# Optimization experiments

Measured on AMD Instinct MI355X. Metric: run time of the kernel, lower is better.

The kernel has to match this reference:

```python
import jax, jax.numpy as jnp
import numpy as np

N, H, E, A, T = 50000, 128, 800000, 16, 4


def setup_inputs() -> dict:
    key = jax.random.key(0)
    ks = jax.random.split(key, 12)
    s = 1.0 / np.sqrt(H + A)
    s2 = 1.0 / np.sqrt(H)
    return {
        "h": jax.random.normal(ks[0], (N, H), dtype=jnp.float32),
        "edge_index": jax.random.randint(ks[1], (2, E), 0, N, dtype=jnp.int32),
        "edge_type": jax.random.randint(ks[2], (E,), 0, T, dtype=jnp.int32),
        "edge_attr": jax.random.normal(ks[3], (E, A), dtype=jnp.float32),
        # per-edge-type 2-layer MLP params
        "W1": jax.random.uniform(ks[4], (T, H + A, H), minval=-s, maxval=s, dtype=jnp.float32),
        "b1": jax.random.uniform(ks[5], (T, H), minval=-s, maxval=s, dtype=jnp.float32),
        "W2": jax.random.uniform(ks[6], (T, H, H), minval=-s2, maxval=s2, dtype=jnp.float32),
        "b2": jax.random.uniform(ks[7], (T, H), minval=-s2, maxval=s2, dtype=jnp.float32),
        # GRUCell params (torch layout: [3H, H] with gate order r, z, n)
        "w_ih": jax.random.uniform(ks[8], (3 * H, H), minval=-s2, maxval=s2, dtype=jnp.float32),
        "w_hh": jax.random.uniform(ks[9], (3 * H, H), minval=-s2, maxval=s2, dtype=jnp.float32),
        "b_ih": jax.random.uniform(ks[10], (3 * H,), minval=-s2, maxval=s2, dtype=jnp.float32),
        "b_hh": jax.random.uniform(ks[11], (3 * H,), minval=-s2, maxval=s2, dtype=jnp.float32),
    }


def reference(h, edge_index, edge_type, edge_attr, W1, b1, W2, b2, w_ih, w_hh, b_ih, b_hh):
    src, dst = edge_index[0], edge_index[1]
    h_in = jnp.concatenate([h[src], edge_attr], axis=-1)  # [E, H+A]
    # per-edge-type MLP; loop over small fixed num_edge_types, mask-select
    m = jnp.zeros((h_in.shape[0], H), dtype=h.dtype)
    for t in range(T):
        mt = jax.nn.relu(h_in @ W1[t] + b1[t]) @ W2[t] + b2[t]  # [E, H]
        m = jnp.where((edge_type == t)[:, None], mt, m)
    # scatter-add messages to destination nodes
    msg = jax.ops.segment_sum(m, dst, num_segments=h.shape[0])  # [N, H]
    # GRUCell(msg, h) with torch gate order r, z, n
    gi = msg @ w_ih.T + b_ih  # [N, 3H]
    gh = h @ w_hh.T + b_hh
    i_r, i_z, i_n = jnp.split(gi, 3, axis=-1)
    h_r, h_z, h_n = jnp.split(gh, 3, axis=-1)
    r = jax.nn.sigmoid(i_r + h_r)
    z = jax.nn.sigmoid(i_z + h_z)
    n = jnp.tanh(i_n + r * h_n)
    return (1.0 - z) * n + z * h
```

## Files before the change

### kernel.cpp

```cpp
#include <hip/hip_runtime.h>
#include <stdint.h>

#define Hh 128
#define Aa 16
#define Tt 4
#define K1 144
#define K1P 160
#define W1T_LD 168
#define WG_LD  136

typedef float f32x4 __attribute__((ext_vector_type(4)));
typedef __bf16 bf16x8 __attribute__((ext_vector_type(8)));
typedef unsigned short u16x8 __attribute__((ext_vector_type(8)));
typedef unsigned short u16x4 __attribute__((ext_vector_type(4)));

static __device__ __forceinline__ unsigned short f2bf(float f) {
    unsigned u = __builtin_bit_cast(unsigned, f);
    u += 0x7fffu + ((u >> 16) & 1u);
    return (unsigned short)(u >> 16);
}

static __device__ __forceinline__ float bf2f(unsigned short u) {
    return __builtin_bit_cast(float, (unsigned)u << 16);
}

static __device__ __forceinline__ bf16x8 zero_bf8() {
    u16x8 z = {0, 0, 0, 0, 0, 0, 0, 0};
    return __builtin_bit_cast(bf16x8, z);
}

__global__ void cast_all_kernel(
    const float* __restrict__ h, const float* __restrict__ ea,
    const float* __restrict__ wih, const float* __restrict__ whh,
    unsigned short* __restrict__ h_bf, unsigned short* __restrict__ ebf,
    unsigned short* __restrict__ wihb, unsigned short* __restrict__ whhb,
    int n0, int n1, int n2, int n3)
{
    int i = blockIdx.x * blockDim.x + threadIdx.x;
    if (i >= n3) return;
    const float* s; unsigned short* d; int off;
    if (i < n0)      { s = h;   d = h_bf; off = i; }
    else if (i < n1) { s = ea;  d = ebf;  off = i - n0; }
    else if (i < n2) { s = wih; d = wihb; off = i - n1; }
    else             { s = whh; d = whhb; off = i - n2; }
    f32x4 v = *(const f32x4*)(s + (size_t)off * 4);
    u16x4 o;
    o[0] = f2bf(v[0]); o[1] = f2bf(v[1]); o[2] = f2bf(v[2]); o[3] = f2bf(v[3]);
    *(u16x4*)(d + (size_t)off * 4) = o;
}

__global__ void w1t_kernel(const float* __restrict__ W1, unsigned short* __restrict__ W1Tbf) {
    __shared__ float tile[16][129];
    const int b = blockIdx.x;
    const int t = b / 10, kb = b % 10;
    const int k0 = kb * 16;
    const int tid = threadIdx.x;
    for (int e = tid; e < 16 * 128; e += 256) {
        int k = e >> 7, n = e & 127;
        tile[k][n] = (k0 + k < K1) ? W1[((size_t)t * K1 + k0 + k) * Hh + n] : 0.f;
    }
    __syncthreads();
    for (int e = tid; e < 128 * 16; e += 256) {
        int n = e >> 4, kk = e & 15;
        W1Tbf[((size_t)t * Hh + n) * K1P + k0 + kk] = f2bf(tile[kk][n]);
    }
}

__global__ void w2t_kernel(const float* __restrict__ W2, unsigned short* __restrict__ W2Tbf) {
    __shared__ float tile[16][129];
    const int b = blockIdx.x;
    const int t = b >> 3, kb = b & 7;
    const int k0 = kb * 16;
    const int tid = threadIdx.x;
    for (int e = tid; e < 16 * 128; e += 256) {
        int k = e >> 7, n = e & 127;
        tile[k][n] = W2[((size_t)t * Hh + k0 + k) * Hh + n];
    }
    __syncthreads();
    for (int e = tid; e < 128 * 16; e += 256) {
        int n = e >> 4, kk = e & 15;
        W2Tbf[((size_t)t * Hh + n) * Hh + k0 + kk] = f2bf(tile[kk][n]);
    }
}

__global__ void hist_kernel(const int* __restrict__ et, const int* __restrict__ eidx,
                            int E, int N, int* __restrict__ cnt, unsigned* __restrict__ rank) {
    for (int i = blockIdx.x * blockDim.x + threadIdx.x; i < E; i += gridDim.x * blockDim.x) {
        rank[i] = (unsigned)atomicAdd(&cnt[et[i] * N + eidx[E + i]], 1);
    }
}

__global__ void scanA_kernel(const int* __restrict__ deg2, int nb, int* __restrict__ bsum) {
    __shared__ int red[256];
    const int t = threadIdx.x;
    const int i0 = blockIdx.x * 1024 + t * 4;
    int s = 0;
    #pragma unroll
    for (int j = 0; j < 4; j++) if (i0 + j < nb) s += deg2[i0 + j];
    red[t] = s; __syncthreads();
    for (int d = 128; d > 0; d >>= 1) {
        if (t < d) red[t] += red[t + d];
        __syncthreads();
    }
    if (t == 0) bsum[blockIdx.x] = red[0];
}

__global__ void scanB_kernel(int* __restrict__ bsum, int nblocks,
                             int* __restrict__ rowptrD, int fourN, int E) {
    __shared__ int ts[512];
    const int t = threadIdx.x;
    int v = (t < nblocks) ? bsum[t] : 0;
    ts[t] = v; __syncthreads();
    for (int d = 1; d < 512; d <<= 1) {
        int x = (t >= d) ? ts[t - d] : 0;
        __syncthreads();
        ts[t] += x;
        __syncthreads();
    }
    if (t < nblocks) bsum[t] = ts[t] - v;
    if (t == 0) rowptrD[fourN] = E;
}

__global__ void scanC_kernel(int* __restrict__ cur, int nb,
                             const int* __restrict__ bsum, int* __restrict__ rowptrD) {
    __shared__ int ts[256];
    const int t = threadIdx.x;
    const int i0 = blockIdx.x * 1024 + t * 4;
    int v[4];
    #pragma unroll
    for (int j = 0; j < 4; j++) v[j] = (i0 + j < nb) ? cur[i0 + j] : 0;
    int s = v[0] + v[1] + v[2] + v[3];
    ts[t] = s; __syncthreads();
    for (int d = 1; d < 256; d <<= 1) {
        int x = (t >= d) ? ts[t - d] : 0;
        __syncthreads();
        ts[t] += x;
        __syncthreads();
    }
    int run = bsum[blockIdx.x] + ts[t] - s;
    #pragma unroll
    for (int j = 0; j < 4; j++) {
        if (i0 + j < nb) {
            rowptrD[i0 + j] = run;
            cur[i0 + j] = run;
            run += v[j];
        }
    }
}

__global__ void fill2_kernel(const int* __restrict__ et, const int* __restrict__ eidx,
                             int E, int N, const int* __restrict__ binstart,
                             const unsigned* __restrict__ rank, int2* __restrict__ rec) {
    for (int i = blockIdx.x * blockDim.x + threadIdx.x; i < E; i += gridDim.x * blockDim.x) {
        int posD = binstart[et[i] * N + eidx[E + i]] + (int)rank[i];
        rec[posD] = make_int2(eidx[i], i);
    }
}

__global__ __launch_bounds__(512) void l1_kernel(
    const unsigned short* __restrict__ h_bf, const int2* __restrict__ rec,
    const unsigned short* __restrict__ ebf, const unsigned short* __restrict__ W1Tbf,
    const float* __restrict__ b1, const int* __restrict__ rowptrD,
    unsigned short* __restrict__ Yg, int N)
{
    __shared__ unsigned short W1T[128 * W1T_LD];
    __shared__ float b1s[128];
    const int tid = threadIdx.x;

    int rem = blockIdx.x, t = 0, tstart = 0, tend = 0;
    for (; t < Tt; t++) {
        tstart = rowptrD[t * N];
        tend = rowptrD[(t + 1) * N];
        int ntt = (tend - tstart + 255) >> 8;
        if (rem < ntt) break;
        rem -= ntt;
    }
    if (t == Tt) return;

    for (int idx = tid; idx < (Hh * K1P) / 8; idx += 512) {
        int n = idx / 20, c = (idx % 20) * 8;
        *(u16x8*)&W1T[n * W1T_LD + c] =
            *(const u16x8*)&W1Tbf[((size_t)t * Hh + n) * K1P + c];
    }
    if (tid < 128) b1s[tid] = b1[t * Hh + tid];
    __syncthreads();

    const int w = tid >> 6, lane = tid & 63;
    const int l15 = lane & 15, q = lane >> 4;
    const int tl = tend - 1;

    const int p0 = tstart + rem * 256 + w * 32;
    const int pa = p0 + l15, pb = p0 + 16 + l15;
    const bool va = pa < tend, vb = pb < tend;
    const int2 ra = rec[min(pa, tl)];
    const int2 rb = rec[min(pb, tl)];
    const unsigned short* __restrict__ hA = h_bf + (size_t)ra.x * Hh;
    const unsigned short* __restrict__ hB = h_bf + (size_t)rb.x * Hh;

    f32x4 acc[8][2];
    #pragma unroll
    for (int mt = 0; mt < 8; mt++) {
        acc[mt][0] = (f32x4){0.f, 0.f, 0.f, 0.f};
        acc[mt][1] = (f32x4){0.f, 0.f, 0.f, 0.f};
    }

    #pragma unroll
    for (int ks = 0; ks < 5; ks++) {
        const int k0 = ks * 32;
        bf16x8 fb_a, fb_b;
        if (ks < 4) {
            fb_a = __builtin_bit_cast(bf16x8, *(const u16x8*)(hA + k0 + q * 8));
            fb_b = __builtin_bit_cast(bf16x8, *(const u16x8*)(hB + k0 + q * 8));
        } else if (q < 2) {
            fb_a = __builtin_bit_cast(bf16x8, *(const u16x8*)(ebf + (size_t)ra.y * Aa + q * 8));
            fb_b = __builtin_bit_cast(bf16x8, *(const u16x8*)(ebf + (size_t)rb.y * Aa + q * 8));
        } else {
            fb_a = zero_bf8();
            fb_b = zero_bf8();
        }
        #pragma unroll
        for (int mt = 0; mt < 8; mt++) {
            bf16x8 fa = *(const bf16x8*)&W1T[(mt * 16 + l15) * W1T_LD + k0 + q * 8];
            acc[mt][0] = __builtin_amdgcn_mfma_f32_16x16x32_bf16(fa, fb_a, acc[mt][0], 0, 0, 0);
            acc[mt][1] = __builtin_amdgcn_mfma_f32_16x16x32_bf16(fa, fb_b, acc[mt][1], 0, 0, 0);
        }
    }

    #pragma unroll
    for (int g = 0; g < 2; g++) {
        if (g ? vb : va) {
            unsigned short* __restrict__ o = Yg + (size_t)(g ? pb : pa) * Hh + q * 4;
            #pragma unroll
            for (int mt = 0; mt < 8; mt++) {
                f32x4 bias = *(const f32x4*)&b1s[mt * 16 + q * 4];
                u16x4 y;
                #pragma unroll
                for (int i = 0; i < 4; i++) {
                    float v = acc[mt][g][i] + bias[i];
                    y[i] = f2bf(v > 0.f ? v : 0.f);
                }
                *(u16x4*)(o + mt * 16) = y;
            }
        }
    }
}

__global__ __launch_bounds__(256) void zgemm_kernel(
    const unsigned short* __restrict__ Yg, const int* __restrict__ rowptrD,
    const unsigned short* __restrict__ W2Tbf, const float* __restrict__ b2,
    unsigned short* __restrict__ msgb, int N)
{
    __shared__ unsigned short W2T[128 * WG_LD];
    __shared__ float b2s[512];
    __shared__ int cntS[4 * 64];
    const int tid = threadIdx.x;
    const int w = tid >> 6, lane = tid & 63;
    const int l15 = lane & 15, q = lane >> 4;
    const int nodebase = blockIdx.x * 64 + w * 16;
    const int nA = min(nodebase + l15, N - 1);

    b2s[tid] = b2[tid];
    b2s[tid + 256] = b2[tid + 256];

    f32x4 acc[8];
    #pragma unroll
    for (int ct = 0; ct < 8; ct++) acc[ct] = (f32x4){0.f, 0.f, 0.f, 0.f};

    for (int t = 0; t < Tt; t++) {
        __syncthreads();
        for (int idx = tid; idx < (Hh * Hh) / 8; idx += 256) {
            int n = idx >> 4, c = (idx & 15) * 8;
            *(u16x8*)&W2T[n * WG_LD + c] =
                *(const u16x8*)&W2Tbf[((size_t)t * Hh + n) * Hh + c];
        }
        __syncthreads();

        const int seg = rowptrD[(size_t)t * N + nA];
        const int len = rowptrD[(size_t)t * N + nA + 1] - seg;
        cntS[w * 64 + t * 16 + l15] = len;

        float asum[32];
        #pragma unroll
        for (int i = 0; i < 32; i++) asum[i] = 0.f;
        for (int j = 0; j < len; j++) {
            const unsigned short* __restrict__ yr = Yg + (size_t)(seg + j) * Hh;
            #pragma unroll
            for (int ks = 0; ks < 4; ks++) {
                u16x8 yv = *(const u16x8*)(yr + ks * 32 + q * 8);
                #pragma unroll
                for (int e = 0; e < 8; e++) asum[ks * 8 + e] += bf2f(yv[e]);
            }
        }

        #pragma unroll
        for (int ks = 0; ks < 4; ks++) {
            u16x8 fr;
            #pragma unroll
            for (int e = 0; e < 8; e++) fr[e] = f2bf(asum[ks * 8 + e]);
            bf16x8 fa = __builtin_bit_cast(bf16x8, fr);
            #pragma unroll
            for (int ct = 0; ct < 8; ct++) {
                bf16x8 fb = *(const bf16x8*)&W2T[(ct * 16 + l15) * WG_LD + ks * 32 + q * 8];
                acc[ct] = __builtin_amdgcn_mfma_f32_16x16x32_bf16(fa, fb, acc[ct], 0, 0, 0);
            }
        }
    }
    __syncthreads();

    #pragma unroll
    for (int ct = 0; ct < 8; ct++) {
        const int c = ct * 16 + l15;
        #pragma unroll
        for (int i = 0; i < 4; i++) {
            int node = nodebase + q * 4 + i;
            if (node < N) {
                float bias = 0.f;
                #pragma unroll
                for (int t = 0; t < Tt; t++)
                    bias += (float)cntS[w * 64 + t * 16 + q * 4 + i] * b2s[t * 128 + c];
                msgb[(size_t)node * Hh + c] = f2bf(acc[ct][i] + bias);
            }
        }
    }
}

__global__ __launch_bounds__(512) void gru_kernel(
    const float* __restrict__ h, const unsigned short* __restrict__ h_bf,
    const unsigned short* __restrict__ msgb,
    const unsigned short* __restrict__ wihb, const unsigned short* __restrict__ whhb,
    const float* __restrict__ b_ih, const float* __restrict__ b_hh,
    float* __restrict__ out, int N)
{
    __shared__ unsigned short Wg[128 * WG_LD];
    const int tid = threadIdx.x;
    const int lane = tid & 63;
    const int l15 = lane & 15, q = lane >> 4;
    const int w = tid >> 6;
    const int nodebase = blockIdx.x * 128 + w * 16;
    const int nA = min(nodebase + l15, N - 1);

    bf16x8 fm[4], fh[4];
    #pragma unroll
    for (int ks = 0; ks < 4; ks++) {
        fm[ks] = __builtin_bit_cast(bf16x8, *(const u16x8*)(msgb + (size_t)nA * Hh + ks * 32 + q * 8));
        fh[ks] = __builtin_bit_cast(bf16x8, *(const u16x8*)(h_bf + (size_t)nA * Hh + ks * 32 + q * 8));
    }

    u16x8 pre[4];
    const int so = tid >> 4, sk = (tid & 15) * 8;
    auto loadg = [&](const unsigned short* __restrict__ Ws, int gate) {
        #pragma unroll
        for (int i = 0; i < 4; i++)
            pre[i] = *(const u16x8*)&Ws[(size_t)gate * Hh * Hh + (size_t)(so + i * 32) * Hh + sk];
    };
    auto commit = [&]() {
        __syncthreads();
        #pragma unroll
        for (int i = 0; i < 4; i++)
            *(u16x8*)&Wg[(so + i * 32) * WG_LD + sk] = pre[i];
        __syncthreads();
    };
    auto matmul = [&](f32x4* acc, const bf16x8* fa) {
        #pragma unroll
        for (int ks = 0; ks < 4; ks++) {
            #pragma unroll
            for (int ct = 0; ct < 8; ct++) {
                bf16x8 fb = *(const bf16x8*)&Wg[(ct * 16 + l15) * WG_LD + ks * 32 + q * 8];
                acc[ct] = __builtin_amdgcn_mfma_f32_16x16x32_bf16(fa[ks], fb, acc[ct], 0, 0, 0);
            }
        }
    };

    f32x4 gr[8], gin[8], ghn[8];
    #pragma unroll
    for (int ct = 0; ct < 8; ct++) {
        gr[ct] = (f32x4){0.f, 0.f, 0.f, 0.f};
        gin[ct] = (f32x4){0.f, 0.f, 0.f, 0.f};
        ghn[ct] = (f32x4){0.f, 0.f, 0.f, 0.f};
    }

    loadg(wihb, 0);
    commit(); loadg(whhb, 0); matmul(gr, fm);
    commit(); loadg(wihb, 2); matmul(gr, fh);
    commit(); loadg(whhb, 2); matmul(gin, fm);
    commit(); loadg(wihb, 1); matmul(ghn, fh);

    #pragma unroll
    for (int ct = 0; ct < 8; ct++) {
        const int c = ct * 16 + l15;
        float bir = b_ih[c], bhr = b_hh[c];
        float bin = b_ih[256 + c], bhn = b_hh[256 + c];
        #pragma unroll
        for (int i = 0; i < 4; i++) {
            float rv = 1.f / (1.f + __expf(-(gr[ct][i] + bir + bhr)));
            gin[ct][i] = gin[ct][i] + bin + rv * (ghn[ct][i] + bhn);
        }
    }
    #pragma unroll
    for (int ct = 0; ct < 8; ct++) gr[ct] = (f32x4){0.f, 0.f, 0.f, 0.f};

    commit(); loadg(whhb, 1); matmul(gr, fm);
    commit();                 matmul(gr, fh);

    #pragma unroll
    for (int ct = 0; ct < 8; ct++) {
        const int c = ct * 16 + l15;
        float biz = b_ih[128 + c], bhz = b_hh[128 + c];
        #pragma unroll
        for (int i = 0; i < 4; i++) {
            int node = nodebase + q * 4 + i;
            if (node < N) {
                float zv = 1.f / (1.f + __expf(-(gr[ct][i] + biz + bhz)));
                float e2 = __expf(-2.f * gin[ct][i]);
                float nv = (1.f - e2) / (1.f + e2);
                float hv = h[(size_t)node * Hh + c];
                out[(size_t)node * Hh + c] = (1.f - zv) * nv + zv * hv;
            }
        }
    }
}

static inline size_t align256(size_t x) { return (x + 255) & ~(size_t)255; }

extern "C" void kernel_launch(void* const* d_in, const int* in_sizes, int n_in,
                              void* d_out, int out_size, void* d_ws, size_t ws_size,
                              hipStream_t stream)
{
    const float* h     = (const float*)d_in[0];
    const int*   eidx  = (const int*)d_in[1];
    const int*   et    = (const int*)d_in[2];
    const float* eattr = (const float*)d_in[3];
    const float* W1    = (const float*)d_in[4];
    const float* b1    = (const float*)d_in[5];
    const float* W2    = (const float*)d_in[6];
    const float* b2    = (const float*)d_in[7];
    const float* w_ih  = (const float*)d_in[8];
    const float* w_hh  = (const float*)d_in[9];
    const float* b_ih  = (const float*)d_in[10];
    const float* b_hh  = (const float*)d_in[11];

    const int N = in_sizes[0] / Hh;
    const int E = in_sizes[1] / 2;
    const int nb = 4 * N;
    const int sblocks = (nb + 1023) / 1024;

    char* p = (char*)d_ws;
    unsigned short* msgb = (unsigned short*)p; p += align256((size_t)N * Hh * sizeof(unsigned short));
    unsigned short* Yg = (unsigned short*)p;   p += align256((size_t)E * Hh * sizeof(unsigned short));
    int2* rec = (int2*)p;               p += align256((size_t)E * sizeof(int2));
    unsigned* rank = (unsigned*)p;      p += align256((size_t)E * sizeof(unsigned));
    int* rowptrD = (int*)p;             p += align256(((size_t)4 * N + 1) * sizeof(int));
    int* cur = (int*)p;                 p += align256((size_t)nb * sizeof(int));
    int* bsum = (int*)p;                p += align256(1024 * sizeof(int));
    unsigned short* h_bf = (unsigned short*)p; p += align256((size_t)N * Hh * sizeof(unsigned short));
    unsigned short* ebf = (unsigned short*)p;  p += align256((size_t)E * Aa * sizeof(unsigned short));
    unsigned short* W1Tbf = (unsigned short*)p; p += align256((size_t)Tt * Hh * K1P * sizeof(unsigned short));
    unsigned short* W2Tbf = (unsigned short*)p; p += align256((size_t)Tt * Hh * Hh * sizeof(unsigned short));
    unsigned short* wihb = (unsigned short*)p; p += align256((size_t)3 * Hh * Hh * sizeof(unsigned short));
    unsigned short* whhb = (unsigned short*)p; p += align256((size_t)3 * Hh * Hh * sizeof(unsigned short));

    hipMemsetAsync(cur, 0, (size_t)nb * sizeof(int), stream);

    {
        int n4h = N * Hh / 4, n4e = E * Aa / 4, n4g = 3 * Hh * Hh / 4;
        int c0 = n4h, c1 = c0 + n4e, c2 = c1 + n4g, c3 = c2 + n4g;
        cast_all_kernel<<<(c3 + 255) / 256, 256, 0, stream>>>(
            h, eattr, w_ih, w_hh, h_bf, ebf, wihb, whhb, c0, c1, c2, c3);
    }
    w1t_kernel<<<Tt * 10, 256, 0, stream>>>(W1, W1Tbf);
    w2t_kernel<<<Tt * 8, 256, 0, stream>>>(W2, W2Tbf);

    hist_kernel<<<1024, 256, 0, stream>>>(et, eidx, E, N, cur, rank);
    scanA_kernel<<<sblocks, 256, 0, stream>>>(cur, nb, bsum);
    scanB_kernel<<<1, 512, 0, stream>>>(bsum, sblocks, rowptrD, 4 * N, E);
    scanC_kernel<<<sblocks, 256, 0, stream>>>(cur, nb, bsum, rowptrD);
    fill2_kernel<<<1024, 256, 0, stream>>>(et, eidx, E, N, cur, rank, rec);

    int l1grid = E / 256 + Tt + 1;
    l1_kernel<<<l1grid, 512, 0, stream>>>(h_bf, rec, ebf, W1Tbf, b1, rowptrD, Yg, N);
    zgemm_kernel<<<(N + 63) / 64, 256, 0, stream>>>(Yg, rowptrD, W2Tbf, b2, msgb, N);

    int gblocks = (N + 127) / 128;
    gru_kernel<<<gblocks, 512, 0, stream>>>(h, h_bf, msgb, wihb, whhb, b_ih, b_hh, (float*)d_out, N);
}
```

Before: 432.7 us.

## Merge cast and weight-transpose kernels; prefetch next Y row in segment sum

```diff
diff --git a/kernel.cpp b/kernel.cpp
--- a/kernel.cpp
+++ b/kernel.cpp
@@ -29,57 +29,63 @@
     return __builtin_bit_cast(bf16x8, z);
 }
 
-__global__ void cast_all_kernel(
+__global__ void prep_kernel(
     const float* __restrict__ h, const float* __restrict__ ea,
     const float* __restrict__ wih, const float* __restrict__ whh,
+    const float* __restrict__ W1, const float* __restrict__ W2,
     unsigned short* __restrict__ h_bf, unsigned short* __restrict__ ebf,
     unsigned short* __restrict__ wihb, unsigned short* __restrict__ whhb,
-    int n0, int n1, int n2, int n3)
+    unsigned short* __restrict__ W1Tbf, unsigned short* __restrict__ W2Tbf,
+    int n0, int n1, int n2, int n3, int castBlocks)
 {
-    int i = blockIdx.x * blockDim.x + threadIdx.x;
-    if (i >= n3) return;
-    const float* s; unsigned short* d; int off;
-    if (i < n0)      { s = h;   d = h_bf; off = i; }
-    else if (i < n1) { s = ea;  d = ebf;  off = i - n0; }
-    else if (i < n2) { s = wih; d = wihb; off = i - n1; }
-    else             { s = whh; d = whhb; off = i - n2; }
-    f32x4 v = *(const f32x4*)(s + (size_t)off * 4);
-    u16x4 o;
-    o[0] = f2bf(v[0]); o[1] = f2bf(v[1]); o[2] = f2bf(v[2]); o[3] = f2bf(v[3]);
-    *(u16x4*)(d + (size_t)off * 4) = o;
-}
-
-__global__ void w1t_kernel(const float* __restrict__ W1, unsigned short* __restrict__ W1Tbf) {
     __shared__ float tile[16][129];
-    const int b = blockIdx.x;
-    const int t = b / 10, kb = b % 10;
-    const int k0 = kb * 16;
     const int tid = threadIdx.x;
-    for (int e = tid; e < 16 * 128; e += 256) {
-        int k = e >> 7, n = e & 127;
-        tile[k][n] = (k0 + k < K1) ? W1[((size_t)t * K1 + k0 + k) * Hh + n] : 0.f;
-    }
-    __syncthreads();
-    for (int e = tid; e < 128 * 16; e += 256) {
-        int n = e >> 4, kk = e & 15;
-        W1Tbf[((size_t)t * Hh + n) * K1P + k0 + kk] = f2bf(tile[kk][n]);
-    }
-}
-
-__global__ void w2t_kernel(const float* __restrict__ W2, unsigned short* __restrict__ W2Tbf) {
-    __shared__ float tile[16][129];
-    const int b = blockIdx.x;
-    const int t = b >> 3, kb = b & 7;
-    const int k0 = kb * 16;
-    const int tid = threadIdx.x;
-    for (int e = tid; e < 16 * 128; e += 256) {
-        int k = e >> 7, n = e & 127;
-        tile[k][n] = W2[((size_t)t * Hh + k0 + k) * Hh + n];
-    }
-    __syncthreads();
-    for (int e = tid; e < 128 * 16; e += 256) {
-        int n = e >> 4, kk = e & 15;
-        W2Tbf[((size_t)t * Hh + n) * Hh + k0 + kk] = f2bf(tile[kk][n]);
+    int b = blockIdx.x;
+
+    if (b < castBlocks) {
+        int i = b * 256 + tid;
+        if (i >= n3) return;
+        const float* s; unsigned short* d; int off;
+        if (i < n0)      { s = h;   d = h_bf; off = i; }
+        else if (i < n1) { s = ea;  d = ebf;  off = i - n0; }
+        else if (i < n2) { s = wih; d = wihb; off = i - n1; }
+        else             { s = whh; d = whhb; off = i - n2; }
+        f32x4 v = *(const f32x4*)(s + (size_t)off * 4);
+        u16x4 o;
+        o[0] = f2bf(v[0]); o[1] = f2bf(v[1]); o[2] = f2bf(v[2]); o[3] = f2bf(v[3]);
+        *(u16x4*)(d + (size_t)off * 4) = o;
+        return;
+    }
+    b -= castBlocks;
+
+    if (b < Tt * 10) {
+        const int t = b / 10, kb = b % 10;
+        const int k0 = kb * 16;
+        for (int e = tid; e < 16 * 128; e += 256) {
+            int k = e >> 7, n = e & 127;
+            tile[k][n] = (k0 + k < K1) ? W1[((size_t)t * K1 + k0 + k) * Hh + n] : 0.f;
+        }
+        __syncthreads();
+        for (int e = tid; e < 128 * 16; e += 256) {
+            int n = e >> 4, kk = e & 15;
+            W1Tbf[((size_t)t * Hh + n) * K1P + k0 + kk] = f2bf(tile[kk][n]);
+        }
+        return;
+    }
+    b -= Tt * 10;
+
+    {
+        const int t = b >> 3, kb = b & 7;
+        const int k0 = kb * 16;
+        for (int e = tid; e < 16 * 128; e += 256) {
+            int k = e >> 7, n = e & 127;
+            tile[k][n] = W2[((size_t)t * Hh + k0 + k) * Hh + n];
+        }
+        __syncthreads();
+        for (int e = tid; e < 128 * 16; e += 256) {
+            int n = e >> 4, kk = e & 15;
+            W2Tbf[((size_t)t * Hh + n) * Hh + k0 + kk] = f2bf(tile[kk][n]);
+        }
     }
 }
 
@@ -282,13 +288,29 @@
         float asum[32];
         #pragma unroll
         for (int i = 0; i < 32; i++) asum[i] = 0.f;
+
+        const unsigned short* __restrict__ yp = Yg + (size_t)seg * Hh + q * 8;
+        u16x8 cur[4];
+        if (len > 0) {
+            #pragma unroll
+            for (int ks = 0; ks < 4; ks++) cur[ks] = *(const u16x8*)(yp + ks * 32);
+        }
         for (int j = 0; j < len; j++) {
-            const unsigned short* __restrict__ yr = Yg + (size_t)(seg + j) * Hh;
+            u16x8 nxt[4];
+            const bool more = (j + 1 < len);
+            if (more) {
+                const unsigned short* __restrict__ yn = yp + (size_t)(j + 1) * Hh;
+                #pragma unroll
+                for (int ks = 0; ks < 4; ks++) nxt[ks] = *(const u16x8*)(yn + ks * 32);
+            }
             #pragma unroll
             for (int ks = 0; ks < 4; ks++) {
-                u16x8 yv = *(const u16x8*)(yr + ks * 32 + q * 8);
                 #pragma unroll
-                for (int e = 0; e < 8; e++) asum[ks * 8 + e] += bf2f(yv[e]);
+                for (int e = 0; e < 8; e++) asum[ks * 8 + e] += bf2f(cur[ks][e]);
+            }
+            if (more) {
+                #pragma unroll
+                for (int ks = 0; ks < 4; ks++) cur[ks] = nxt[ks];
             }
         }
 
@@ -464,11 +486,11 @@
     {
         int n4h = N * Hh / 4, n4e = E * Aa / 4, n4g = 3 * Hh * Hh / 4;
         int c0 = n4h, c1 = c0 + n4e, c2 = c1 + n4g, c3 = c2 + n4g;
-        cast_all_kernel<<<(c3 + 255) / 256, 256, 0, stream>>>(
-            h, eattr, w_ih, w_hh, h_bf, ebf, wihb, whhb, c0, c1, c2, c3);
-    }
-    w1t_kernel<<<Tt * 10, 256, 0, stream>>>(W1, W1Tbf);
-    w2t_kernel<<<Tt * 8, 256, 0, stream>>>(W2, W2Tbf);
+        int castBlocks = (c3 + 255) / 256;
+        prep_kernel<<<castBlocks + Tt * 10 + Tt * 8, 256, 0, stream>>>(
+            h, eattr, w_ih, w_hh, W1, W2,
+            h_bf, ebf, wihb, whhb, W1Tbf, W2Tbf, c0, c1, c2, c3, castBlocks);
+    }
 
     hist_kernel<<<1024, 256, 0, stream>>>(et, eidx, E, N, cur, rank);
     scanA_kernel<<<sblocks, 256, 0, stream>>>(cur, nb, bsum);
```

New measurement: 437.9 us. No clear change (+1.2%).
